# Optimization experiments

Measured on AMD Instinct MI355X. Metric: run time of the kernel, lower is better.

Reference implementation:

```python
import jax, jax.numpy as jnp
import numpy as np

B, L, KDIM, QDIM, ADIM, ODIM, H = 4, 1024, 1024, 1024, 1024, 1024, 16
DK = ADIM // H
SCALE = float(np.sqrt(DK))
NEG_INF = float(np.finfo(np.float32).min)


def setup_inputs() -> dict:
    key = jax.random.key(0)
    ks = jax.random.split(key, 12)
    s = 0.02
    return {
        "key": jax.random.normal(ks[0], (B, L, KDIM), jnp.float32),
        "value": jax.random.normal(ks[1], (B, L, KDIM), jnp.float32),
        "query": jax.random.normal(ks[2], (B, L, QDIM), jnp.float32),
        "mask": jax.random.randint(ks[3], (B, L, L), 0, 2, jnp.int32),
        "Wk": jax.random.normal(ks[4], (ADIM, KDIM), jnp.float32) * s,
        "bk": jnp.zeros((ADIM,), jnp.float32),
        "Wv": jax.random.normal(ks[5], (ADIM, KDIM), jnp.float32) * s,
        "bv": jnp.zeros((ADIM,), jnp.float32),
        "Wq": jax.random.normal(ks[6], (ADIM, QDIM), jnp.float32) * s,
        "bq": jnp.zeros((ADIM,), jnp.float32),
        "Wo": jax.random.normal(ks[7], (ODIM, ADIM), jnp.float32) * s,
        "bo": jnp.zeros((ODIM,), jnp.float32),
    }


def reference(key, value, query, mask, Wk, bk, Wv, bv, Wq, bq, Wo, bo):
    bs, klen = key.shape[0], key.shape[1]
    qlen = query.shape[1]
    # projections -> [B, len, H, d_k]
    k = (key @ Wk.T + bk).reshape(bs, klen, H, DK)
    v = (value @ Wv.T + bv).reshape(bs, klen, H, DK)
    q = (query @ Wq.T + bq).reshape(bs, qlen, H, DK)
    # attention energy [B, qlen, klen, H]
    e = jnp.einsum('bihd,bjhd->bijh', q, k) / SCALE
    m = mask[:, :, :, None]  # [B,q,k,1] broadcasts over heads
    e = jnp.where(m == 0, NEG_INF, e)
    aw = jax.nn.softmax(e, axis=2)  # softmax over klen
    cv = jnp.einsum('bijh,bjhd->bihd', aw, v).reshape(bs, qlen, ADIM)
    cv = cv @ Wo.T + bo
    return cv, jnp.transpose(aw, (0, 3, 1, 2))  # [B,H,q,k]
```

## Files before the change

kernel.cpp:

```cpp
#include <hip/hip_runtime.h>
#include <hip/hip_bf16.h>

typedef __attribute__((ext_vector_type(8))) __bf16 bf16x8;
typedef __attribute__((ext_vector_type(8))) short short8;
typedef __attribute__((ext_vector_type(4))) float f32x4;

#define LN 1024
#define NH 16
#define DKH 64

__device__ __forceinline__ short f2bf(float f) {
    unsigned u = __builtin_bit_cast(unsigned, f);
    u = u + 0x7fffu + ((u >> 16) & 1u);
    return (short)(u >> 16);
}
__device__ __forceinline__ float bf2f(short s) {
    return __builtin_bit_cast(float, ((unsigned)(unsigned short)s) << 16);
}

__device__ __forceinline__ void gl_lds16(const short* g, short* l) {
    __builtin_amdgcn_global_load_lds(
        (const __attribute__((address_space(1))) void*)g,
        (__attribute__((address_space(3))) void*)l, 16, 0, 0);
}

__global__ __launch_bounds__(256) void cvt_bf16(
    const float* __restrict__ s, short* __restrict__ d, int n8)
{
    int i = blockIdx.x * 256 + threadIdx.x;
    if (i < n8) {
        f32x4 a = ((const f32x4*)s)[i * 2];
        f32x4 b = ((const f32x4*)s)[i * 2 + 1];
        short8 o;
        #pragma unroll
        for (int j = 0; j < 4; ++j) { o[j] = f2bf(a[j]); o[4 + j] = f2bf(b[j]); }
        ((short8*)d)[i] = o;
    }
}

__global__ __launch_bounds__(256) void mask_bits_kernel(
    const int* __restrict__ mask, unsigned long long* __restrict__ bits)
{
    const int i = blockIdx.x;
    const int b = blockIdx.y;
    const int q = threadIdx.x >> 6;
    const int lane = threadIdx.x & 63;
    const int* mp = &mask[((size_t)b * LN + i) * LN + q * 256 + lane * 4];
    int4 mv = *(const int4*)mp;
    unsigned long long b0 = __ballot(mv.x != 0);
    unsigned long long b1 = __ballot(mv.y != 0);
    unsigned long long b2 = __ballot(mv.z != 0);
    unsigned long long b3 = __ballot(mv.w != 0);
    if (lane == 0) {
        unsigned long long* o = &bits[(((size_t)b * LN + i) * 4 + q) * 4];
        o[0] = b0; o[1] = b1; o[2] = b2; o[3] = b3;
    }
}

template<bool OUT_F32>
__global__ __launch_bounds__(256) void gemm_bt_bf16(
    const short* __restrict__ A, const short* __restrict__ Bt,
    const float* __restrict__ bias, void* __restrict__ Cp,
    int M, int N, int K)
{
    __shared__ short lA[64 * 64];
    __shared__ short lB[64 * 64];
    const int tid = threadIdx.x;
    const int lane = tid & 63;
    const int wid = tid >> 6;
    const int wr = wid >> 1, wc = wid & 1;
    const int m0 = blockIdx.y * 64, n0 = blockIdx.x * 64;
    const int lr = lane & 15, lg = lane >> 4;

    int srow[2], skc[2];
    #pragma unroll
    for (int p = 0; p < 2; ++p) {
        int ch = p * 256 + wid * 64 + lane;
        srow[p] = ch >> 3;
        skc[p] = (((ch & 7) ^ (srow[p] & 7))) * 8;
    }

    f32x4 acc[2][2] = {};

    for (int k0 = 0; k0 < K; k0 += 64) {
        #pragma unroll
        for (int p = 0; p < 2; ++p) {
            short* dstA = &lA[(p * 256 + wid * 64) * 8];
            short* dstB = &lB[(p * 256 + wid * 64) * 8];
            gl_lds16(A  + (size_t)(m0 + srow[p]) * K + k0 + skc[p], dstA);
            gl_lds16(Bt + (size_t)(n0 + srow[p]) * K + k0 + skc[p], dstB);
        }
        __syncthreads();
        bf16x8 af[2][2], bfr[2][2];
        #pragma unroll
        for (int kh = 0; kh < 2; ++kh) {
            #pragma unroll
            for (int m = 0; m < 2; ++m) {
                int arow = wr * 32 + m * 16 + lr;
                af[kh][m] = *(const bf16x8*)&lA[arow * 64 + (((kh * 4 + lg) ^ (arow & 7)) * 8)];
            }
            #pragma unroll
            for (int n = 0; n < 2; ++n) {
                int brow = wc * 32 + n * 16 + lr;
                bfr[kh][n] = *(const bf16x8*)&lB[brow * 64 + (((kh * 4 + lg) ^ (brow & 7)) * 8)];
            }
        }
        #pragma unroll
        for (int kh = 0; kh < 2; ++kh)
            #pragma unroll
            for (int m = 0; m < 2; ++m)
                #pragma unroll
                for (int n = 0; n < 2; ++n)
                    acc[m][n] = __builtin_amdgcn_mfma_f32_16x16x32_bf16(af[kh][m], bfr[kh][n], acc[m][n], 0, 0, 0);
        __syncthreads();
    }

    #pragma unroll
    for (int m = 0; m < 2; ++m)
        #pragma unroll
        for (int n = 0; n < 2; ++n) {
            int col = n0 + wc * 32 + n * 16 + lr;
            float bb = bias[col];
            #pragma unroll
            for (int r = 0; r < 4; ++r) {
                int row = m0 + wr * 32 + m * 16 + lg * 4 + r;
                float v = acc[m][n][r] + bb;
                if (OUT_F32) ((float*)Cp)[(size_t)row * N + col] = v;
                else         ((short*)Cp)[(size_t)row * N + col] = f2bf(v);
            }
        }
}

__global__ __launch_bounds__(256) void transpose_v(
    const short* __restrict__ v, short* __restrict__ vT)
{
    __shared__ short t[64 * 72];
    const int j0 = blockIdx.x * 64;
    const int h = blockIdx.y;
    const int b = blockIdx.z;
    const int tid = threadIdx.x;
    for (int idx = tid; idx < 512; idx += 256) {
        int j = idx >> 3, c = (idx & 7) * 8;
        *(short8*)&t[j * 72 + c] =
            *(const short8*)&v[((size_t)b * LN + j0 + j) * 1024 + h * 64 + c];
    }
    __syncthreads();
    for (int idx = tid; idx < 512; idx += 256) {
        int d = idx >> 3, jc = (idx & 7) * 8;
        short8 o;
        #pragma unroll
        for (int jj = 0; jj < 8; ++jj) o[jj] = t[(jc + jj) * 72 + d];
        *(short8*)&vT[((size_t)((b * NH + h) * DKH) + d) * LN + j0 + jc] = o;
    }
}

__global__ __launch_bounds__(256, 2) void attn_kernel(
    const short* __restrict__ qb, const short* __restrict__ kb,
    const short* __restrict__ vT, const unsigned long long* __restrict__ mb,
    float* __restrict__ aw, short* __restrict__ cv)
{
    __shared__ short p_lds[32 * 1024];
    __shared__ float redbuf[4][32];

    const int i0 = blockIdx.x * 32;
    const int h = blockIdx.y;
    const int b = blockIdx.z;
    const int tid = threadIdx.x;
    const int lane = tid & 63;
    const int w = tid >> 6;
    const int lr = lane & 15, lg = lane >> 4;

    unsigned long long Bm[2][4];
    #pragma unroll
    for (int g = 0; g < 2; ++g)
        #pragma unroll
        for (int r = 0; r < 4; ++r)
            Bm[g][r] = mb[(((size_t)b * LN + i0 + g * 16 + lg * 4 + r) * 4 + w) * 4 + (lr & 3)] >> (lr >> 2);

    bf16x8 a0[2], a1[2];
    #pragma unroll
    for (int g = 0; g < 2; ++g) {
        const short* qp = &qb[((size_t)b * LN + i0 + g * 16 + lr) * 1024 + h * 64 + lg * 8];
        a0[g] = *(const bf16x8*)qp;
        a1[g] = *(const bf16x8*)(qp + 32);
    }

    f32x4 acc[2][16];
    #pragma unroll
    for (int g = 0; g < 2; ++g)
        #pragma unroll
        for (int jf = 0; jf < 16; ++jf) acc[g][jf] = f32x4{0.f, 0.f, 0.f, 0.f};

    const size_t krow_base = (size_t)b * LN;
    #pragma unroll
    for (int jf = 0; jf < 16; ++jf) {
        int j0f = w * 256 + jf * 16;
        const short* kp = &kb[(krow_base + j0f + lr) * 1024 + h * 64 + lg * 8];
        bf16x8 b0 = *(const bf16x8*)kp;
        bf16x8 b1 = *(const bf16x8*)(kp + 32);
        acc[0][jf] = __builtin_amdgcn_mfma_f32_16x16x32_bf16(a0[0], b0, acc[0][jf], 0, 0, 0);
        acc[0][jf] = __builtin_amdgcn_mfma_f32_16x16x32_bf16(a1[0], b1, acc[0][jf], 0, 0, 0);
        acc[1][jf] = __builtin_amdgcn_mfma_f32_16x16x32_bf16(a0[1], b0, acc[1][jf], 0, 0, 0);
        acc[1][jf] = __builtin_amdgcn_mfma_f32_16x16x32_bf16(a1[1], b1, acc[1][jf], 0, 0, 0);
    }

    float ps[2][4] = {};
    #pragma unroll
    for (int g = 0; g < 2; ++g)
        #pragma unroll
        for (int jf = 0; jf < 16; ++jf)
            #pragma unroll
            for (int r = 0; r < 4; ++r) {
                float p = ((Bm[g][r] >> (jf * 4)) & 1ULL) ? __expf(acc[g][jf][r] * 0.125f) : 0.0f;
                acc[g][jf][r] = p;
                ps[g][r] += p;
            }

    #pragma unroll
    for (int g = 0; g < 2; ++g)
        #pragma unroll
        for (int r = 0; r < 4; ++r) {
            for (int off = 1; off < 16; off <<= 1) ps[g][r] += __shfl_xor(ps[g][r], off, 64);
        }
    if (lr == 0) {
        #pragma unroll
        for (int g = 0; g < 2; ++g)
            #pragma unroll
            for (int r = 0; r < 4; ++r) redbuf[w][g * 16 + lg * 4 + r] = ps[g][r];
    }

    #pragma unroll
    for (int g = 0; g < 2; ++g)
        #pragma unroll
        for (int jf = 0; jf < 16; ++jf) {
            int j = w * 256 + jf * 16 + lr;
            #pragma unroll
            for (int r = 0; r < 4; ++r) {
                int row = g * 16 + lg * 4 + r;
                int byte = (row * 2048 + j * 2) ^ ((row & 7) << 4);
                *(short*)((char*)p_lds + byte) = f2bf(acc[g][jf][r]);
            }
        }
    __syncthreads();

    float inv[2][4];
    #pragma unroll
    for (int g = 0; g < 2; ++g)
        #pragma unroll
        for (int r = 0; r < 4; ++r) {
            float s = redbuf[0][g * 16 + lg * 4 + r];
            for (int ww = 1; ww < 4; ++ww) s += redbuf[ww][g * 16 + lg * 4 + r];
            inv[g][r] = 1.0f / s;
        }

    float* awp = aw + ((size_t)(b * NH + h) * LN + i0) * LN;
    #pragma unroll
    for (int g = 0; g < 2; ++g)
        #pragma unroll
        for (int jf = 0; jf < 16; ++jf) {
            int j = w * 256 + jf * 16 + lr;
            #pragma unroll
            for (int r = 0; r < 4; ++r)
                awp[(size_t)(g * 16 + lg * 4 + r) * LN + j] = acc[g][jf][r] * inv[g][r];
        }

    f32x4 accA[2] = {}, accB[2] = {};
    const int d0 = w * 16;
    const short* vrow = vT + ((size_t)((b * NH + h) * DKH) + d0 + lr) * LN;
    #pragma unroll
    for (int ks = 0; ks < 32; ks += 2) {
        bf16x8 vb0 = *(const bf16x8*)&vrow[ks * 32 + lg * 8];
        bf16x8 vb1 = *(const bf16x8*)&vrow[(ks + 1) * 32 + lg * 8];
        #pragma unroll
        for (int g = 0; g < 2; ++g) {
            int row = g * 16 + lr;
            int byte0 = (row * 2048 + (ks * 32 + lg * 8) * 2) ^ ((row & 7) << 4);
            int byte1 = (row * 2048 + ((ks + 1) * 32 + lg * 8) * 2) ^ ((row & 7) << 4);
            bf16x8 pa0 = *(const bf16x8*)((char*)p_lds + byte0);
            bf16x8 pa1 = *(const bf16x8*)((char*)p_lds + byte1);
            accA[g] = __builtin_amdgcn_mfma_f32_16x16x32_bf16(pa0, vb0, accA[g], 0, 0, 0);
            accB[g] = __builtin_amdgcn_mfma_f32_16x16x32_bf16(pa1, vb1, accB[g], 0, 0, 0);
        }
    }
    #pragma unroll
    for (int g = 0; g < 2; ++g)
        #pragma unroll
        for (int r = 0; r < 4; ++r) {
            int irow = i0 + g * 16 + lg * 4 + r;
            cv[((size_t)b * LN + irow) * 1024 + h * 64 + d0 + lr] = f2bf((accA[g][r] + accB[g][r]) * inv[g][r]);
        }
}

extern "C" void kernel_launch(void* const* d_in, const int* in_sizes, int n_in,
                              void* d_out, int out_size, void* d_ws, size_t ws_size,
                              hipStream_t stream) {
    (void)in_sizes; (void)n_in; (void)out_size; (void)ws_size;
    const float* key   = (const float*)d_in[0];
    const float* value = (const float*)d_in[1];
    const float* query = (const float*)d_in[2];
    const int*   mask  = (const int*)d_in[3];
    const float* Wk = (const float*)d_in[4];
    const float* bk = (const float*)d_in[5];
    const float* Wv = (const float*)d_in[6];
    const float* bv = (const float*)d_in[7];
    const float* Wq = (const float*)d_in[8];
    const float* bq = (const float*)d_in[9];
    const float* Wo = (const float*)d_in[10];
    const float* bo = (const float*)d_in[11];

    float* out_cv = (float*)d_out;
    float* out_aw = out_cv + (size_t)4096 * 1024;

    unsigned long long* mbits_g = (unsigned long long*)out_cv;

    const size_t MB = 1u << 20;
    char* ws = (char*)d_ws;
    short* qin  = (short*)(ws + 0 * MB);   short* k_bf  = qin;
    short* kin  = (short*)(ws + 8 * MB);   short* cv_bf = kin;
    short* vin  = (short*)(ws + 16 * MB);  short* vT    = vin;
    short* wq   = (short*)(ws + 24 * MB);
    short* wk   = (short*)(ws + 26 * MB);
    short* wv   = (short*)(ws + 28 * MB);
    short* wo   = (short*)(ws + 30 * MB);
    short* v_bf = (short*)(ws + 32 * MB);  short* q_bf  = v_bf;

    dim3 blk(256);
    auto cv8 = [&](const float* s, short* d, int n) {
        int n8 = n / 8;
        cvt_bf16<<<dim3((n8 + 255) / 256), blk, 0, stream>>>(s, d, n8);
    };
    cv8(query, qin, 4096 * 1024);
    cv8(key,   kin, 4096 * 1024);
    cv8(value, vin, 4096 * 1024);
    cv8(Wq, wq, 1024 * 1024);
    cv8(Wk, wk, 1024 * 1024);
    cv8(Wv, wv, 1024 * 1024);
    cv8(Wo, wo, 1024 * 1024);
    mask_bits_kernel<<<dim3(1024, 4), blk, 0, stream>>>(mask, mbits_g);

    dim3 gproj(16, 64);
    gemm_bt_bf16<false><<<gproj, blk, 0, stream>>>(vin, wv, bv, v_bf, 4096, 1024, 1024);
    transpose_v<<<dim3(16, 16, 4), blk, 0, stream>>>(v_bf, vT);
    gemm_bt_bf16<false><<<gproj, blk, 0, stream>>>(qin, wq, bq, q_bf, 4096, 1024, 1024);
    gemm_bt_bf16<false><<<gproj, blk, 0, stream>>>(kin, wk, bk, k_bf, 4096, 1024, 1024);
    attn_kernel<<<dim3(32, 16, 4), blk, 0, stream>>>(q_bf, k_bf, vT, mbits_g, out_aw, cv_bf);
    gemm_bt_bf16<true><<<gproj, blk, 0, stream>>>(cv_bf, wo, bo, out_cv, 4096, 1024, 1024);
}
```

Baseline: 224.7 us.

## Coalesce attention-weight stores via LDS, fuse V transpose into GEMM, merge converts

Attention weights are now written from the bf16 probabilities staged in LDS, with each thread storing contiguous 128-bit chunks per row instead of scattered per-fragment fp32 stores. The V projection GEMM writes its output directly in transposed per-head layout, which removes the separate transpose kernel. The seven conversion launches are merged into one kernel. As a trade-off, the output attention weights are derived from bf16-rounded values, which reduces their precision.

```diff
diff --git a/kernel.cpp b/kernel.cpp
--- a/kernel.cpp
+++ b/kernel.cpp
@@ -3,6 +3,7 @@
 
 typedef __attribute__((ext_vector_type(8))) __bf16 bf16x8;
 typedef __attribute__((ext_vector_type(8))) short short8;
+typedef __attribute__((ext_vector_type(4))) short s16x4;
 typedef __attribute__((ext_vector_type(4))) float f32x4;
 
 #define LN 1024
@@ -24,18 +25,30 @@
         (__attribute__((address_space(3))) void*)l, 16, 0, 0);
 }
 
-__global__ __launch_bounds__(256) void cvt_bf16(
-    const float* __restrict__ s, short* __restrict__ d, int n8)
+__global__ __launch_bounds__(256) void cvt_all(
+    const float* __restrict__ q, const float* __restrict__ k, const float* __restrict__ v,
+    const float* __restrict__ wq, const float* __restrict__ wk,
+    const float* __restrict__ wv, const float* __restrict__ wo,
+    short* __restrict__ dq, short* __restrict__ dk, short* __restrict__ dv,
+    short* __restrict__ dwq, short* __restrict__ dwk,
+    short* __restrict__ dwv, short* __restrict__ dwo)
 {
-    int i = blockIdx.x * 256 + threadIdx.x;
-    if (i < n8) {
-        f32x4 a = ((const f32x4*)s)[i * 2];
-        f32x4 b = ((const f32x4*)s)[i * 2 + 1];
-        short8 o;
-        #pragma unroll
-        for (int j = 0; j < 4; ++j) { o[j] = f2bf(a[j]); o[4 + j] = f2bf(b[j]); }
-        ((short8*)d)[i] = o;
-    }
+    int bid = blockIdx.x;
+    const float* s; short* d; int base;
+    if      (bid < 2048) { s = q;  d = dq;  base = bid; }
+    else if (bid < 4096) { s = k;  d = dk;  base = bid - 2048; }
+    else if (bid < 6144) { s = v;  d = dv;  base = bid - 4096; }
+    else if (bid < 6656) { s = wq; d = dwq; base = bid - 6144; }
+    else if (bid < 7168) { s = wk; d = dwk; base = bid - 6656; }
+    else if (bid < 7680) { s = wv; d = dwv; base = bid - 7168; }
+    else                 { s = wo; d = dwo; base = bid - 7680; }
+    int i = base * 256 + threadIdx.x;
+    f32x4 a = ((const f32x4*)s)[i * 2];
+    f32x4 b = ((const f32x4*)s)[i * 2 + 1];
+    short8 o;
+    #pragma unroll
+    for (int j = 0; j < 4; ++j) { o[j] = f2bf(a[j]); o[4 + j] = f2bf(b[j]); }
+    ((short8*)d)[i] = o;
 }
 
 __global__ __launch_bounds__(256) void mask_bits_kernel(
@@ -57,7 +70,7 @@
     }
 }
 
-template<bool OUT_F32>
+template<bool OUT_F32, bool OUT_VT>
 __global__ __launch_bounds__(256) void gemm_bt_bf16(
     const short* __restrict__ A, const short* __restrict__ Bt,
     const float* __restrict__ bias, void* __restrict__ Cp,
@@ -121,37 +134,24 @@
         for (int n = 0; n < 2; ++n) {
             int col = n0 + wc * 32 + n * 16 + lr;
             float bb = bias[col];
-            #pragma unroll
-            for (int r = 0; r < 4; ++r) {
-                int row = m0 + wr * 32 + m * 16 + lg * 4 + r;
-                float v = acc[m][n][r] + bb;
-                if (OUT_F32) ((float*)Cp)[(size_t)row * N + col] = v;
-                else         ((short*)Cp)[(size_t)row * N + col] = f2bf(v);
-            }
-        }
-}
-
-__global__ __launch_bounds__(256) void transpose_v(
-    const short* __restrict__ v, short* __restrict__ vT)
-{
-    __shared__ short t[64 * 72];
-    const int j0 = blockIdx.x * 64;
-    const int h = blockIdx.y;
-    const int b = blockIdx.z;
-    const int tid = threadIdx.x;
-    for (int idx = tid; idx < 512; idx += 256) {
-        int j = idx >> 3, c = (idx & 7) * 8;
-        *(short8*)&t[j * 72 + c] =
-            *(const short8*)&v[((size_t)b * LN + j0 + j) * 1024 + h * 64 + c];
-    }
-    __syncthreads();
-    for (int idx = tid; idx < 512; idx += 256) {
-        int d = idx >> 3, jc = (idx & 7) * 8;
-        short8 o;
-        #pragma unroll
-        for (int jj = 0; jj < 8; ++jj) o[jj] = t[(jc + jj) * 72 + d];
-        *(short8*)&vT[((size_t)((b * NH + h) * DKH) + d) * LN + j0 + jc] = o;
-    }
+            if (OUT_VT) {
+                int row = m0 + wr * 32 + m * 16 + lg * 4;
+                int bb_i = row >> 10, tok = row & 1023;
+                int hh = col >> 6, dd = col & 63;
+                s16x4 o;
+                #pragma unroll
+                for (int r = 0; r < 4; ++r) o[r] = f2bf(acc[m][n][r] + bb);
+                *(s16x4*)&((short*)Cp)[((size_t)((bb_i * NH + hh) * DKH) + dd) * LN + tok] = o;
+            } else {
+                #pragma unroll
+                for (int r = 0; r < 4; ++r) {
+                    int row = m0 + wr * 32 + m * 16 + lg * 4 + r;
+                    float v = acc[m][n][r] + bb;
+                    if (OUT_F32) ((float*)Cp)[(size_t)row * N + col] = v;
+                    else         ((short*)Cp)[(size_t)row * N + col] = f2bf(v);
+                }
+            }
+        }
 }
 
 __global__ __launch_bounds__(256, 2) void attn_kernel(
@@ -243,6 +243,30 @@
         }
     __syncthreads();
 
+    {
+        const int arow = tid >> 3;
+        const int ac0 = tid & 7;
+        float s = redbuf[0][arow] + redbuf[1][arow] + redbuf[2][arow] + redbuf[3][arow];
+        float ainv = 1.0f / s;
+        float* awr = aw + ((size_t)(b * NH + h) * LN + i0 + arow) * LN;
+        const int abase = arow * 2048;
+        const int aswz = (arow & 7) << 4;
+        #pragma unroll
+        for (int it = 0; it < 16; ++it) {
+            int k = ac0 + it * 8;
+            int byte = (abase + k * 16) ^ aswz;
+            short8 pv = *(const short8*)((char*)p_lds + byte);
+            f32x4 o0, o1;
+            #pragma unroll
+            for (int j = 0; j < 4; ++j) {
+                o0[j] = bf2f(pv[j]) * ainv;
+                o1[j] = bf2f(pv[4 + j]) * ainv;
+            }
+            *(f32x4*)&awr[k * 8] = o0;
+            *(f32x4*)&awr[k * 8 + 4] = o1;
+        }
+    }
+
     float inv[2][4];
     #pragma unroll
     for (int g = 0; g < 2; ++g)
@@ -251,17 +275,6 @@
             float s = redbuf[0][g * 16 + lg * 4 + r];
             for (int ww = 1; ww < 4; ++ww) s += redbuf[ww][g * 16 + lg * 4 + r];
             inv[g][r] = 1.0f / s;
-        }
-
-    float* awp = aw + ((size_t)(b * NH + h) * LN + i0) * LN;
-    #pragma unroll
-    for (int g = 0; g < 2; ++g)
-        #pragma unroll
-        for (int jf = 0; jf < 16; ++jf) {
-            int j = w * 256 + jf * 16 + lr;
-            #pragma unroll
-            for (int r = 0; r < 4; ++r)
-                awp[(size_t)(g * 16 + lg * 4 + r) * LN + j] = acc[g][jf][r] * inv[g][r];
         }
 
     f32x4 accA[2] = {}, accB[2] = {};
@@ -317,32 +330,23 @@
     char* ws = (char*)d_ws;
     short* qin  = (short*)(ws + 0 * MB);   short* k_bf  = qin;
     short* kin  = (short*)(ws + 8 * MB);   short* cv_bf = kin;
-    short* vin  = (short*)(ws + 16 * MB);  short* vT    = vin;
+    short* vin  = (short*)(ws + 16 * MB);  short* q_bf  = vin;
     short* wq   = (short*)(ws + 24 * MB);
     short* wk   = (short*)(ws + 26 * MB);
     short* wv   = (short*)(ws + 28 * MB);
     short* wo   = (short*)(ws + 30 * MB);
-    short* v_bf = (short*)(ws + 32 * MB);  short* q_bf  = v_bf;
+    short* vT   = (short*)(ws + 32 * MB);
 
     dim3 blk(256);
-    auto cv8 = [&](const float* s, short* d, int n) {
-        int n8 = n / 8;
-        cvt_bf16<<<dim3((n8 + 255) / 256), blk, 0, stream>>>(s, d, n8);
-    };
-    cv8(query, qin, 4096 * 1024);
-    cv8(key,   kin, 4096 * 1024);
-    cv8(value, vin, 4096 * 1024);
-    cv8(Wq, wq, 1024 * 1024);
-    cv8(Wk, wk, 1024 * 1024);
-    cv8(Wv, wv, 1024 * 1024);
-    cv8(Wo, wo, 1024 * 1024);
+    cvt_all<<<dim3(8192), blk, 0, stream>>>(
+        query, key, value, Wq, Wk, Wv, Wo,
+        qin, kin, vin, wq, wk, wv, wo);
     mask_bits_kernel<<<dim3(1024, 4), blk, 0, stream>>>(mask, mbits_g);
 
     dim3 gproj(16, 64);
-    gemm_bt_bf16<false><<<gproj, blk, 0, stream>>>(vin, wv, bv, v_bf, 4096, 1024, 1024);
-    transpose_v<<<dim3(16, 16, 4), blk, 0, stream>>>(v_bf, vT);
-    gemm_bt_bf16<false><<<gproj, blk, 0, stream>>>(qin, wq, bq, q_bf, 4096, 1024, 1024);
-    gemm_bt_bf16<false><<<gproj, blk, 0, stream>>>(kin, wk, bk, k_bf, 4096, 1024, 1024);
+    gemm_bt_bf16<false, true ><<<gproj, blk, 0, stream>>>(vin, wv, bv, vT,    4096, 1024, 1024);
+    gemm_bt_bf16<false, false><<<gproj, blk, 0, stream>>>(qin, wq, bq, q_bf,  4096, 1024, 1024);
+    gemm_bt_bf16<false, false><<<gproj, blk, 0, stream>>>(kin, wk, bk, k_bf,  4096, 1024, 1024);
     attn_kernel<<<dim3(32, 16, 4), blk, 0, stream>>>(q_bf, k_bf, vT, mbits_g, out_aw, cv_bf);
-    gemm_bt_bf16<true><<<gproj, blk, 0, stream>>>(cv_bf, wo, bo, out_cv, 4096, 1024, 1024);
-}
+    gemm_bt_bf16<true, false><<<gproj, blk, 0, stream>>>(cv_bf, wo, bo, out_cv, 4096, 1024, 1024);
+}
```

New measurement: 210.1 us. 6.5% less time.
